# Kernel tuning notes

Measured on AMD Instinct MI355X. Metric: run time of the kernel, lower is better.

The kernel has to match this reference:

```python
import jax, jax.numpy as jnp
import numpy as np

PH, PW = 7, 7          # output_size
GRID = 2               # sampling_ratio
SCALES = (0.25, 0.125, 0.0625, 0.03125)  # 2^round(log2(feat/img)) per level
LVL_MIN, LVL_MAX = 2, 5                  # -log2(scales[0]), -log2(scales[-1])
CANON_SCALE, CANON_LVL = 224.0, 4.0
EPS = 1e-6


def setup_inputs() -> dict:
    key = jax.random.key(0)
    ks = jax.random.split(key, 6)
    B, C = 2, 256
    sizes = [(200, 200), (100, 100), (50, 50), (25, 25)]
    inp = {f"feat{i}": jax.random.normal(ks[i], (B, C, h, w), jnp.float32)
           for i, (h, w) in enumerate(sizes)}
    Nb = 256
    # boxes in 800x800 image coords, x1y1 + positive wh so 0<=x1<x2, 0<=y1<y2
    xy = jax.random.uniform(ks[4], (B, Nb, 2), jnp.float32, 0.0, 700.0)
    wh = jax.random.uniform(ks[5], (B, Nb, 2), jnp.float32, 32.0, 512.0)
    inp["boxes"] = jnp.concatenate([xy, xy + wh], axis=-1)
    return inp


def _roi_align_level(feat, b_idx, rois, scale):
    """torchvision roi_align, aligned=False. feat [B,C,H,W], rois [R,4] -> [R,C,PH,PW]."""
    H, W = feat.shape[2], feat.shape[3]
    x1 = rois[:, 0] * scale
    y1 = rois[:, 1] * scale
    x2 = rois[:, 2] * scale
    y2 = rois[:, 3] * scale
    roi_w = jnp.maximum(x2 - x1, 1.0)
    roi_h = jnp.maximum(y2 - y1, 1.0)
    bin_w = roi_w / PW
    bin_h = roi_h / PH
    # sub-bin sampling offsets: (bin + (i+0.5)/grid) for each bin, flattened [PH*GRID]
    gy = (jnp.arange(PH, dtype=jnp.float32)[:, None]
          + (jnp.arange(GRID, dtype=jnp.float32)[None, :] + 0.5) / GRID).reshape(-1)
    gx = (jnp.arange(PW, dtype=jnp.float32)[:, None]
          + (jnp.arange(GRID, dtype=jnp.float32)[None, :] + 0.5) / GRID).reshape(-1)
    ys = y1[:, None] + gy[None, :] * bin_h[:, None]   # [R, PH*G]
    xs = x1[:, None] + gx[None, :] * bin_w[:, None]   # [R, PW*G]
    y = ys[:, :, None]                                 # [R, PH*G, 1]
    x = xs[:, None, :]                                 # [R, 1, PW*G]
    valid = (y >= -1.0) & (y <= H) & (x >= -1.0) & (x <= W)
    yc = jnp.clip(y, 0.0, H - 1)
    xc = jnp.clip(x, 0.0, W - 1)
    yl = jnp.floor(yc).astype(jnp.int32)
    xl = jnp.floor(xc).astype(jnp.int32)
    yh = jnp.minimum(yl + 1, H - 1)
    xh = jnp.minimum(xl + 1, W - 1)
    ly = yc - yl.astype(yc.dtype)
    lx = xc - xl.astype(xc.dtype)
    hy = 1.0 - ly
    hx = 1.0 - lx
    b = b_idx[:, None, None]

    def gather(yi, xi):
        # advanced indexing with slice in channel dim -> [R, PH*G, PW*G, C]
        return feat[b, :, yi, xi]

    val = ((hy * hx)[..., None] * gather(yl, xl)
           + (hy * lx)[..., None] * gather(yl, xh)
           + (ly * hx)[..., None] * gather(yh, xl)
           + (ly * lx)[..., None] * gather(yh, xh))
    val = jnp.where(valid[..., None], val, 0.0)
    R, C = rois.shape[0], feat.shape[1]
    # average over the GRIDxGRID sampling points of each bin
    val = val.reshape(R, PH, GRID, PW, GRID, C).mean(axis=(2, 4))  # [R,PH,PW,C]
    return jnp.transpose(val, (0, 3, 1, 2))                        # [R,C,PH,PW]


def reference(feat0, feat1, feat2, feat3, boxes):
    feats = [feat0, feat1, feat2, feat3]
    B, Nb = boxes.shape[0], boxes.shape[1]
    rois = boxes.reshape(-1, 4)                               # convert_to_roi_format
    b_idx = jnp.repeat(jnp.arange(B), Nb)
    # LevelMapper (FPN eq. 1)
    s = jnp.sqrt(jnp.maximum((rois[:, 2] - rois[:, 0]) * (rois[:, 3] - rois[:, 1]), 0.0))
    lvl = jnp.floor(CANON_LVL + jnp.log2(s / CANON_SCALE + EPS))
    lvl = jnp.clip(lvl, LVL_MIN, LVL_MAX).astype(jnp.int32) - LVL_MIN  # [R] in [0,3]
    out = jnp.zeros((rois.shape[0], feats[0].shape[1], PH, PW), feats[0].dtype)
    for l, (f, sc) in enumerate(zip(feats, SCALES)):
        pooled = _roi_align_level(f, b_idx, rois, sc)
        out = jnp.where((lvl == l)[:, None, None, None], pooled, out)
    return out
```

## Files before the change

kernel.cpp:

```cpp
#include <hip/hip_runtime.h>


#define PHW 49
#define NCHUNK 8
#define CH 32
#define PSIZE 1024

#define BARRIER_KEEP_VMCNT()                                   \
    do {                                                       \
        asm volatile("s_waitcnt lgkmcnt(0)" ::: "memory");     \
        __builtin_amdgcn_s_barrier();                          \
    } while (0)

__global__ __launch_bounds__(256, 5) void msroi_kernel(
    const float* __restrict__ f0, const float* __restrict__ f1,
    const float* __restrict__ f2, const float* __restrict__ f3,
    const float* __restrict__ boxes, float* __restrict__ out)
{
    const int C = 256, Nb = 256;
    const int r = blockIdx.x;
    const int chunk = blockIdx.y;
    const int tid = threadIdx.x;
    const int b = r / Nb;

    const int bin = tid >> 2;
    const int q   = tid & 3;
    const bool active = bin < PHW;

    const float x1b = boxes[r * 4 + 0];
    const float y1b = boxes[r * 4 + 1];
    const float x2b = boxes[r * 4 + 2];
    const float y2b = boxes[r * 4 + 3];
    const float area = fmaxf((x2b - x1b) * (y2b - y1b), 0.0f);
    const float s = sqrtf(area);
    float lv = floorf(4.0f + log2f(s / 224.0f + 1e-6f));
    lv = fminf(fmaxf(lv, 2.0f), 5.0f);
    const int lvl = (int)lv - 2;

    const float* feat;
    int H, W;
    float scale;
    switch (lvl) {
        case 0:  feat = f0; H = 200; W = 200; scale = 0.25f;    break;
        case 1:  feat = f1; H = 100; W = 100; scale = 0.125f;   break;
        case 2:  feat = f2; H = 50;  W = 50;  scale = 0.0625f;  break;
        default: feat = f3; H = 25;  W = 25;  scale = 0.03125f; break;
    }
    const int HW = H * W;

    const float x1 = x1b * scale, y1 = y1b * scale;
    const float x2 = x2b * scale, y2 = y2b * scale;
    const float roi_w = fmaxf(x2 - x1, 1.0f);
    const float roi_h = fmaxf(y2 - y1, 1.0f);
    const float bin_w = roi_w * (1.0f / 7.0f);
    const float bin_h = roi_h * (1.0f / 7.0f);

    const float ys0 = fminf(fmaxf(y1 + 0.25f * bin_h, 0.0f), (float)(H - 1));
    const float ys1 = fminf(fmaxf(y1 + 6.75f * bin_h, 0.0f), (float)(H - 1));
    const float xs0 = fminf(fmaxf(x1 + 0.25f * bin_w, 0.0f), (float)(W - 1));
    const float xs1 = fminf(fmaxf(x1 + 6.75f * bin_w, 0.0f), (float)(W - 1));
    const int row0 = (int)floorf(ys0);
    const int row1 = min((int)floorf(ys1) + 1, H - 1);
    const int col0 = (int)floorf(xs0);
    const int col1 = min((int)floorf(xs1) + 1, W - 1);
    const int prows = row1 - row0 + 1;
    const int pcols = col1 - col0 + 1;
    const int psize = prows * pcols;
    const int wstride = W - pcols;
    const float inv_pcols = 1.0f / (float)pcols;

    int goff[4];
#pragma unroll
    for (int k = 0; k < 4; ++k) {
        const int e = tid + k * 256;
        const int ec = min(e, psize - 1);
        const int rr = (int)floorf(((float)ec + 0.5f) * inv_pcols);
        goff[k] = ec + rr * wstride;
    }

    int   offs[4];
    float wts[4];
    {
        const int bb = active ? bin : 0;
        const int ph = bb / 7;
        const int pw = bb - ph * 7;
        const int iy = q >> 1, ix = q & 1;
        const float gy = (float)ph + ((float)iy + 0.5f) * 0.5f;
        const float gx = (float)pw + ((float)ix + 0.5f) * 0.5f;
        const float y = y1 + gy * bin_h;
        const float x = x1 + gx * bin_w;
        const bool valid = (y >= -1.0f) && (y <= (float)H) &&
                           (x >= -1.0f) && (x <= (float)W);
        const float yc = fminf(fmaxf(y, 0.0f), (float)(H - 1));
        const float xc = fminf(fmaxf(x, 0.0f), (float)(W - 1));
        const int yl = (int)floorf(yc);
        const int xl = (int)floorf(xc);
        const int yh = min(yl + 1, H - 1);
        const int xh = min(xl + 1, W - 1);
        const float ly = yc - (float)yl;
        const float lx = xc - (float)xl;
        const float hy = 1.0f - ly, hx = 1.0f - lx;
        const float m = valid ? 0.25f : 0.0f;
        const int ry0 = (yl - row0) * pcols, ry1 = (yh - row0) * pcols;
        const int cx0 = xl - col0, cx1 = xh - col0;
        offs[0] = ry0 + cx0;  wts[0] = hy * hx * m;
        offs[1] = ry0 + cx1;  wts[1] = hy * lx * m;
        offs[2] = ry1 + cx0;  wts[2] = ly * hx * m;
        offs[3] = ry1 + cx1;  wts[3] = ly * lx * m;
    }

    __shared__ float4 lds4[2][PSIZE];

    const int cbase = chunk * CH;
    const float* __restrict__ fch =
        feat + (size_t)(b * C + cbase) * HW + (row0 * W + col0);
    float* __restrict__ outp =
        out + (size_t)r * C * PHW + (size_t)cbase * PHW;

    float4 bufA[4], bufB[4];

#define LOADR(BUF, CCV)                                                    \
    do {                                                                   \
        const float* __restrict__ g0 = fch + (size_t)((CCV) + 0) * HW;     \
        const float* __restrict__ g1 = fch + (size_t)((CCV) + 1) * HW;     \
        const float* __restrict__ g2 = fch + (size_t)((CCV) + 2) * HW;     \
        const float* __restrict__ g3 = fch + (size_t)((CCV) + 3) * HW;     \
        _Pragma("unroll")                                                  \
        for (int k = 0; k < 4; ++k) {                                      \
            BUF[k].x = g0[goff[k]];                                        \
            BUF[k].y = g1[goff[k]];                                        \
            BUF[k].z = g2[goff[k]];                                        \
            BUF[k].w = g3[goff[k]];                                        \
        }                                                                  \
    } while (0)

#define WRITELDS(SL, BUF)                                                  \
    do {                                                                   \
        _Pragma("unroll")                                                  \
        for (int k = 0; k < 4; ++k)                                        \
            lds4[SL][tid + k * 256] = BUF[k];                              \
    } while (0)

#define COMPUTE(SL, CCV)                                                   \
    do {                                                                   \
        if (active) {                                                      \
            float4 a = make_float4(0.0f, 0.0f, 0.0f, 0.0f);                \
            _Pragma("unroll")                                              \
            for (int j = 0; j < 4; ++j) {                                  \
                const float4 v = lds4[SL][offs[j]];                        \
                a.x += wts[j] * v.x;                                       \
                a.y += wts[j] * v.y;                                       \
                a.z += wts[j] * v.z;                                       \
                a.w += wts[j] * v.w;                                       \
            }                                                              \
            a.x += __shfl_xor(a.x, 1); a.y += __shfl_xor(a.y, 1);          \
            a.z += __shfl_xor(a.z, 1); a.w += __shfl_xor(a.w, 1);          \
            a.x += __shfl_xor(a.x, 2); a.y += __shfl_xor(a.y, 2);          \
            a.z += __shfl_xor(a.z, 2); a.w += __shfl_xor(a.w, 2);          \
            const float vout = (q == 0) ? a.x : (q == 1) ? a.y             \
                             : (q == 2) ? a.z : a.w;                       \
            outp[(size_t)((CCV) + q) * PHW + bin] = vout;                  \
        }                                                                  \
    } while (0)

    LOADR(bufA, 0);
    LOADR(bufB, 4);
    WRITELDS(0, bufA);
    LOADR(bufA, 8);
    BARRIER_KEEP_VMCNT();

#pragma unroll
    for (int i = 0; i < 8; ++i) {
        const int cur = i & 1, nxt = cur ^ 1;
        COMPUTE(cur, i * 4);
        if (i < 7) {
            if (i & 1) {
                WRITELDS(nxt, bufA);
                if (i + 3 < 8) LOADR(bufA, (i + 3) * 4);
            } else {
                WRITELDS(nxt, bufB);
                if (i + 3 < 8) LOADR(bufB, (i + 3) * 4);
            }
        }
        BARRIER_KEEP_VMCNT();
    }
#undef LOADR
#undef WRITELDS
#undef COMPUTE
}

extern "C" void kernel_launch(void* const* d_in, const int* in_sizes, int n_in,
                              void* d_out, int out_size, void* d_ws, size_t ws_size,
                              hipStream_t stream) {
    const float* f0 = (const float*)d_in[0];
    const float* f1 = (const float*)d_in[1];
    const float* f2 = (const float*)d_in[2];
    const float* f3 = (const float*)d_in[3];
    const float* boxes = (const float*)d_in[4];
    float* out = (float*)d_out;

    const int R = in_sizes[4] / 4;
    dim3 grid(R, NCHUNK);
    msroi_kernel<<<grid, 256, 0, stream>>>(f0, f1, f2, f3, boxes, out);
}
```

Before: 180.1 us.

## Stage ROI feature patches with direct global-to-LDS loads instead of registers

```diff
diff --git a/kernel.cpp b/kernel.cpp
--- a/kernel.cpp
+++ b/kernel.cpp
@@ -4,15 +4,9 @@
 #define PHW 49
 #define NCHUNK 8
 #define CH 32
-#define PSIZE 1024
+#define SLABQ 960
 
-#define BARRIER_KEEP_VMCNT()                                   \
-    do {                                                       \
-        asm volatile("s_waitcnt lgkmcnt(0)" ::: "memory");     \
-        __builtin_amdgcn_s_barrier();                          \
-    } while (0)
-
-__global__ __launch_bounds__(256, 5) void msroi_kernel(
+__global__ __launch_bounds__(256) void msroi_kernel(
     const float* __restrict__ f0, const float* __restrict__ f1,
     const float* __restrict__ f2, const float* __restrict__ f3,
     const float* __restrict__ boxes, float* __restrict__ out)
@@ -69,13 +63,16 @@
     const int wstride = W - pcols;
     const float inv_pcols = 1.0f / (float)pcols;
 
-    int goff[4];
+    const int smax = (psize + 63) >> 6;
+    int gsrc[15];
 #pragma unroll
-    for (int k = 0; k < 4; ++k) {
-        const int e = tid + k * 256;
-        const int ec = min(e, psize - 1);
-        const int rr = (int)floorf(((float)ec + 0.5f) * inv_pcols);
-        goff[k] = ec + rr * wstride;
+    for (int k = 0; k < 15; ++k) {
+        const int sl = k * 256 + tid;
+        const int sc = min(sl, 4 * psize - 1);
+        const int e  = sc >> 2;
+        const int cl = sc & 3;
+        const int rr = (int)floorf(((float)e + 0.5f) * inv_pcols);
+        gsrc[k] = (cl * HW + e + rr * wstride) * 4;
     }
 
     int   offs[4];
@@ -109,7 +106,7 @@
         offs[3] = ry1 + cx1;  wts[3] = ly * lx * m;
     }
 
-    __shared__ float4 lds4[2][PSIZE];
+    __shared__ float4 lds4[2][SLABQ];
 
     const int cbase = chunk * CH;
     const float* __restrict__ fch =
@@ -117,28 +114,23 @@
     float* __restrict__ outp =
         out + (size_t)r * C * PHW + (size_t)cbase * PHW;
 
-    float4 bufA[4], bufB[4];
+    const int wbase4 = (tid & 192) * 4;
 
-#define LOADR(BUF, CCV)                                                    \
+#define STAGE(SL, CC)                                                      \
     do {                                                                   \
-        const float* __restrict__ g0 = fch + (size_t)((CCV) + 0) * HW;     \
-        const float* __restrict__ g1 = fch + (size_t)((CCV) + 1) * HW;     \
-        const float* __restrict__ g2 = fch + (size_t)((CCV) + 2) * HW;     \
-        const float* __restrict__ g3 = fch + (size_t)((CCV) + 3) * HW;     \
+        const char* gb = (const char*)fch + (size_t)(CC) * HW * 4;         \
+        char* lb = (char*)(&lds4[SL][0]);                                  \
         _Pragma("unroll")                                                  \
-        for (int k = 0; k < 4; ++k) {                                      \
-            BUF[k].x = g0[goff[k]];                                        \
-            BUF[k].y = g1[goff[k]];                                        \
-            BUF[k].z = g2[goff[k]];                                        \
-            BUF[k].w = g3[goff[k]];                                        \
+        for (int k = 0; k < 15; ++k) {                                     \
+            if (k < smax) {                                                \
+                __builtin_amdgcn_global_load_lds(                          \
+                    (const __attribute__((address_space(1))) void*)        \
+                        (gb + gsrc[k]),                                    \
+                    (__attribute__((address_space(3))) void*)              \
+                        (lb + k * 1024 + wbase4),                          \
+                    4, 0, 0);                                              \
+            }                                                              \
         }                                                                  \
-    } while (0)
-
-#define WRITELDS(SL, BUF)                                                  \
-    do {                                                                   \
-        _Pragma("unroll")                                                  \
-        for (int k = 0; k < 4; ++k)                                        \
-            lds4[SL][tid + k * 256] = BUF[k];                              \
     } while (0)
 
 #define COMPUTE(SL, CCV)                                                   \
@@ -163,29 +155,17 @@
         }                                                                  \
     } while (0)
 
-    LOADR(bufA, 0);
-    LOADR(bufB, 4);
-    WRITELDS(0, bufA);
-    LOADR(bufA, 8);
-    BARRIER_KEEP_VMCNT();
+    STAGE(0, 0);
+    __syncthreads();
 
 #pragma unroll
     for (int i = 0; i < 8; ++i) {
-        const int cur = i & 1, nxt = cur ^ 1;
+        const int cur = i & 1;
+        if (i < 7) STAGE(cur ^ 1, (i + 1) * 4);
         COMPUTE(cur, i * 4);
-        if (i < 7) {
-            if (i & 1) {
-                WRITELDS(nxt, bufA);
-                if (i + 3 < 8) LOADR(bufA, (i + 3) * 4);
-            } else {
-                WRITELDS(nxt, bufB);
-                if (i + 3 < 8) LOADR(bufB, (i + 3) * 4);
-            }
-        }
-        BARRIER_KEEP_VMCNT();
+        __syncthreads();
     }
-#undef LOADR
-#undef WRITELDS
+#undef STAGE
 #undef COMPUTE
 }
 
```

Result: slower. 184.0 us (+2.1%).
